# Optimization experiments

Hardware: AMD Instinct MI355X
Metric: run time of the kernel (lower is better)

## Reference

```python
import jax, jax.numpy as jnp
import numpy as np

PS = 8          # patch_size
NF = 64         # num_feat
HEADS = 1
HW = 64         # hard-coded spatial size (Fold output_size=(64,64))
DIM = PS * PS * NF          # 4096
HID = DIM // HEADS          # 4096
NPATCH = (HW // PS) ** 2    # 64


def conv2d(x, w, b, groups=1):
    # x: [N,C,H,W], w: [O, C//groups, 3, 3], padding=1 stride=1 == SAME
    y = jax.lax.conv_general_dilated(
        x, w, window_strides=(1, 1), padding='SAME',
        dimension_numbers=('NCHW', 'OIHW', 'NCHW'),
        feature_group_count=groups)
    return y + b[None, :, None, None]


def unfold(x):
    # nn.Unfold(kernel=PS, stride=PS): [N,C,64,64] -> [N, C*PS*PS, NPATCH]
    N, C = x.shape[0], x.shape[1]
    g = HW // PS
    x = x.reshape(N, C, g, PS, g, PS)          # [N,C,gh,pi,gw,pj]
    x = x.transpose(0, 1, 3, 5, 2, 4)          # [N,C,pi,pj,gh,gw]
    return x.reshape(N, C * PS * PS, g * g)


def fold(y):
    # nn.Fold(output=(64,64), kernel=PS, stride=PS): inverse of unfold (non-overlapping)
    N = y.shape[0]
    g = HW // PS
    y = y.reshape(N, NF, PS, PS, g, g)         # [N,C,pi,pj,gh,gw]
    y = y.transpose(0, 1, 4, 2, 5, 3)          # [N,C,gh,pi,gw,pj]
    return y.reshape(N, NF, HW, HW)


def setup_inputs() -> dict:
    key = jax.random.key(0)
    ks = jax.random.split(key, 9)
    b, t = 4, 16
    x = jax.random.normal(ks[0], (b, t, NF, HW, HW), dtype=jnp.float32)
    s_dw = 1.0 / np.sqrt(9.0)          # depthwise: fan_in = 1*3*3
    s_fc = 1.0 / np.sqrt(NF * 9.0)     # full conv: fan_in = 64*3*3
    qw = jax.random.normal(ks[1], (NF, 1, 3, 3), jnp.float32) * s_dw
    qb = jax.random.normal(ks[2], (NF,), jnp.float32) * 0.01
    kw = jax.random.normal(ks[3], (NF, 1, 3, 3), jnp.float32) * s_dw
    kb = jax.random.normal(ks[4], (NF,), jnp.float32) * 0.01
    vw = jax.random.normal(ks[5], (NF, NF, 3, 3), jnp.float32) * s_fc
    vb = jax.random.normal(ks[6], (NF,), jnp.float32) * 0.01
    cw = jax.random.normal(ks[7], (NF, NF, 3, 3), jnp.float32) * s_fc
    cb = jax.random.normal(ks[8], (NF,), jnp.float32) * 0.01
    return {"x": x, "qw": qw, "qb": qb, "kw": kw, "kb": kb,
            "vw": vw, "vb": vb, "cw": cw, "cb": cb}


def reference(x, qw, qb, kw, kb, vw, vb, cw, cb):
    b, t, c, h, w = x.shape
    H, d, n = HEADS, HID, NPATCH
    xf = x.reshape(b * t, c, h, w)
    q = conv2d(xf, qw, qb, groups=NF)   # depthwise
    k = conv2d(xf, kw, kb, groups=NF)   # depthwise
    v = conv2d(xf, vw, vb)              # full conv
    # unfold -> [b,t,H,d,n] -> [b,H,d,t*n]
    def to_tokens(z):
        z = unfold(z).reshape(b, t, H, d, n)
        return z.transpose(0, 2, 3, 1, 4).reshape(b, H, d, t * n)
    uq, uk, uv = to_tokens(q), to_tokens(k), to_tokens(v)
    attn = jnp.einsum('bhdi,bhdj->bhij', uq, uk) * (d ** -0.5)
    attn = jax.nn.softmax(attn, axis=-1)
    ax = jnp.einsum('bhij,bhdj->bhid', attn, uv)          # [b,H,t*n,d]
    ax = ax.reshape(b, H, t, n, d).transpose(0, 2, 1, 4, 3)  # [b,t,H,d,n]
    ax = ax.reshape(b * t, DIM, n)
    feat = fold(ax)                                        # [b*t,C,64,64]
    out = conv2d(feat, cw, cb).reshape(x.shape)
    return out + x
```

## Files before the change

### kernel.cpp

```cpp
#include <hip/hip_runtime.h>

typedef unsigned short u16;
typedef unsigned int   u32;

typedef __bf16 bf16_t;
typedef bf16_t bf16x8 __attribute__((ext_vector_type(8)));
typedef float  f32x4  __attribute__((ext_vector_type(4)));

__device__ __forceinline__ float bf2f(u16 h) { return __uint_as_float(((u32)h) << 16); }
__device__ __forceinline__ u16 f2bf(float f) {
    u32 u = __float_as_uint(f);
    u32 r = u + 0x7fffu + ((u >> 16) & 1u);
    return (u16)(r >> 16);
}
__device__ __forceinline__ void unpack2(u32 v, float& a, float& b) {
    a = __uint_as_float(v << 16);
    b = __uint_as_float(v & 0xffff0000u);
}


__global__ __launch_bounds__(256) void dwconv_qk(
    const float* __restrict__ x, const float* __restrict__ qw, const float* __restrict__ qb,
    const float* __restrict__ kw, const float* __restrict__ kb,
    u16* __restrict__ qtok, u16* __restrict__ ktok)
{
    __shared__ float ts[64][65];
    int img = blockIdx.x >> 6, c = blockIdx.x & 63;
    int tid = threadIdx.x;
    const float* xp = x + ((size_t)((img << 6) + c) << 12);
    #pragma unroll
    for (int i = 0; i < 4; i++) {
        int p = i * 1024 + tid * 4;
        int r = p >> 6, col = p & 63;
        float4 v = *(const float4*)(xp + p);
        ts[r][col] = v.x; ts[r][col + 1] = v.y; ts[r][col + 2] = v.z; ts[r][col + 3] = v.w;
    }
    float qwv[9], kwv[9];
    #pragma unroll
    for (int i = 0; i < 9; i++) { qwv[i] = qw[c * 9 + i]; kwv[i] = kw[c * 9 + i]; }
    float qbb = qb[c], kbb = kb[c];
    __syncthreads();

    int r = tid >> 2, q = tid & 3;
    int b = img >> 4, t = img & 15;
    int gh = r >> 3, pr = r & 7;
    size_t base = (((size_t)(b << 10) + (t << 6) + (gh << 3)) << 12) + (c << 6) + (pr << 3);

    #pragma unroll
    for (int s = 0; s < 2; s++) {
        int gw = q * 2 + s, w0 = gw << 3;
        float qa[8], ka[8];
        #pragma unroll
        for (int i = 0; i < 8; i++) { qa[i] = qbb; ka[i] = kbb; }
        #pragma unroll
        for (int ky = 0; ky < 3; ky++) {
            int hh = r + ky - 1;
            if (hh < 0 || hh > 63) continue;
            float xr[10];
            #pragma unroll
            for (int cc = 0; cc < 10; cc++) {
                int ww = w0 - 1 + cc;
                xr[cc] = (ww < 0 || ww > 63) ? 0.f : ts[hh][ww];
            }
            #pragma unroll
            for (int kx = 0; kx < 3; kx++) {
                float wq = qwv[ky * 3 + kx], wk = kwv[ky * 3 + kx];
                #pragma unroll
                for (int i = 0; i < 8; i++) {
                    qa[i] += xr[i + kx] * wq;
                    ka[i] += xr[i + kx] * wk;
                }
            }
        }
        union { u16 h8[8]; uint4 u; } pq, pk;
        #pragma unroll
        for (int i = 0; i < 8; i++) { pq.h8[i] = f2bf(qa[i]); pk.h8[i] = f2bf(ka[i]); }
        size_t o = base + ((size_t)gw << 12);
        *(uint4*)&qtok[o] = pq.u;
        *(uint4*)&ktok[o] = pk.u;
    }
}

__global__ __launch_bounds__(256) void nchw_to_nhwc(
    const float* __restrict__ x, u16* __restrict__ xb)
{
    __shared__ float ts[64][65];
    int img = blockIdx.x >> 6, h = blockIdx.x & 63;
    int tid = threadIdx.x;
    const float* xp = x + ((size_t)img << 18) + (h << 6);
    int c = tid >> 2, wg = (tid & 3) << 4;
    #pragma unroll
    for (int i = 0; i < 4; i++) {
        float4 v = *(const float4*)(xp + ((size_t)c << 12) + wg + i * 4);
        ts[c][wg + i * 4 + 0] = v.x; ts[c][wg + i * 4 + 1] = v.y;
        ts[c][wg + i * 4 + 2] = v.z; ts[c][wg + i * 4 + 3] = v.w;
    }
    __syncthreads();
    int w = tid >> 2, cg = (tid & 3) << 4;
    union { u16 h8[8]; uint4 u; } p0, p1;
    #pragma unroll
    for (int m = 0; m < 8; m++) {
        p0.h8[m] = f2bf(ts[cg + m][w]);
        p1.h8[m] = f2bf(ts[cg + 8 + m][w]);
    }
    u16* dst = xb + (((((size_t)img << 6) + h) << 6) + w) * 64 + cg;
    *(uint4*)dst       = p0.u;
    *(uint4*)(dst + 8) = p1.u;
}

__global__ __launch_bounds__(256) void weight_prep2(
    const float* __restrict__ vw, const float* __restrict__ cw, u16* __restrict__ wt)
{
    int e = blockIdx.x * 256 + threadIdx.x;
    if (e >= 73728) return;
    int half = e >= 36864;
    int e2 = e - (half ? 36864 : 0);
    int tap = e2 >> 12;
    int kbg = (e2 >> 9) & 7;
    int cout = (e2 >> 3) & 63;
    int s = e2 & 7;
    int cin = (kbg << 3) + s;
    const float* src = half ? cw : vw;
    wt[e] = f2bf(src[((cout << 6) + cin) * 9 + tap]);
}

template<bool IS_C>
__global__ __launch_bounds__(256, 2) void conv_mfma(
    const u16* __restrict__ xb, const u16* __restrict__ wt,
    const float* __restrict__ bias, const float* __restrict__ xres,
    u16* __restrict__ vt, float* __restrict__ out)
{
    __shared__ u16 xs[21120];
    __shared__ u16 wl[18432];

    int tid = threadIdx.x, lane = tid & 63, wv = tid >> 6;
    int img = blockIdx.x >> 3, rowblk = blockIdx.x & 7;
    int h0 = rowblk << 3;
    int r16 = lane & 15, kb = lane >> 4;

    const uint4 z4 = make_uint4(0, 0, 0, 0);
    for (int i = tid; i < 80; i += 256) {
        int r = i >> 3, k = i & 7;
        *(uint4*)&xs[r * 2112 + 2048 + k * 8] = z4;
    }
    if (rowblk == 0)
        for (int i = tid; i < 264; i += 256) *(uint4*)&xs[i * 8] = z4;
    if (rowblk == 7)
        for (int i = tid; i < 264; i += 256) *(uint4*)&xs[9 * 2112 + i * 8] = z4;

    int pxoff[4][3];
    #pragma unroll
    for (int g = 0; g < 4; g++) {
        #pragma unroll
        for (int dx = 0; dx < 3; dx++) {
            int cc = g * 16 + r16 + dx - 1;
            int off;
            if (cc < 0)        off = 2048 + kb * 8;
            else if (cc >= 64) off = 2080 + kb * 8;
            else               off = (cc >> 4) * 512 + kb * 128 + (cc & 15) * 8;
            pxoff[g][dx] = off;
        }
    }

    const u16* xb_i = xb + ((size_t)img << 18);

    f32x4 acc[4][8] = {};

    for (int c0 = 0; c0 < 64; c0 += 32) {
        __syncthreads();
        #pragma unroll
        for (int k = 0; k < 10; k++) {
            int i = wv + (k << 2);
            int r = i >> 2, g = i & 3;
            int h = h0 + r - 1;
            if (h >= 0 && h < 64) {
                const u16* src = xb_i + (size_t)(((h << 6) + (g << 4) + r16) << 6)
                                 + c0 + (kb << 3);
                u16* dst = xs + r * 2112 + g * 512;
                __builtin_amdgcn_global_load_lds(
                    (const __attribute__((address_space(1))) u32*)src,
                    (__attribute__((address_space(3))) u32*)dst, 16, 0, 0);
            }
        }
        #pragma unroll
        for (int tp = 0; tp < 9; tp++) {
            const u16* srcw = wt + tp * 4096 + (c0 << 6) + tid * 8;
            u16* dstw = wl + tp * 2048 + (wv << 9);
            __builtin_amdgcn_global_load_lds(
                (const __attribute__((address_space(1))) u32*)srcw,
                (__attribute__((address_space(3))) u32*)dstw, 16, 0, 0);
        }
        __syncthreads();

        #pragma unroll
        for (int dy = 0; dy < 3; dy++) {
            #pragma unroll
            for (int dx = 0; dx < 3; dx++) {
                int tap = dy * 3 + dx;
                bf16x8 af[4];
                #pragma unroll
                for (int m = 0; m < 4; m++)
                    af[m] = *(const bf16x8*)&wl[tap * 2048 + (kb << 9)
                                                + (((m << 4) + r16) << 3)];
                #pragma unroll
                for (int nf = 0; nf < 8; nf++) {
                    int rowb = ((wv << 1) + (nf >> 2) + dy) * 2112;
                    bf16x8 bv = *(const bf16x8*)&xs[rowb + pxoff[nf & 3][dx]];
                    #pragma unroll
                    for (int m = 0; m < 4; m++)
                        acc[m][nf] = __builtin_amdgcn_mfma_f32_16x16x32_bf16(
                            af[m], bv, acc[m][nf], 0, 0, 0);
                }
            }
        }
    }

    int b = img >> 4, t = img & 15;
    if constexpr (!IS_C) {
        __syncthreads();
        u16* wbuf = xs + (wv << 12);
        int j0 = (t << 6) + (rowblk << 3);
        #pragma unroll
        for (int mh = 0; mh < 2; mh++) {
            #pragma unroll
            for (int mm = 0; mm < 2; mm++) {
                int m = mh * 2 + mm;
                #pragma unroll
                for (int q = 0; q < 4; q++) {
                    int cm = mm * 16 + (kb << 2) + q;
                    float bvs = bias[mh * 32 + cm];
                    #pragma unroll
                    for (int nf = 0; nf < 8; nf++) {
                        int lrL = nf >> 2;
                        int pc  = r16 & 7;
                        int gw  = ((nf & 3) << 1) | (r16 >> 3);
                        wbuf[(((cm << 1) | lrL) << 6) + (pc << 3) + gw] =
                            f2bf(acc[m][nf][q] + bvs);
                    }
                }
            }
            #pragma unroll
            for (int it = 0; it < 8; it++) {
                int cid = it * 64 + lane;
                int cm  = cid >> 4;
                int lrL = (cid >> 3) & 1;
                int pc  = cid & 7;
                int lr  = (wv << 1) | lrL;
                int cout = mh * 32 + cm;
                int dd  = (((lr << 3) | pc) << 6) | cout;
                uint4 val = *(uint4*)&wbuf[cid << 3];
                *(uint4*)&vt[(((size_t)((b << 12) + dd)) << 10) + j0] = val;
            }
            if (mh == 0) __syncthreads();
        }
    } else {
        #pragma unroll
        for (int m = 0; m < 4; m++) {
            #pragma unroll
            for (int q = 0; q < 4; q++) {
                int cout = (m << 4) + (kb << 2) + q;
                float bvs = bias[cout];
                #pragma unroll
                for (int nf = 0; nf < 8; nf++) {
                    int lr = (wv << 1) + (nf >> 2);
                    int w = (nf & 3) * 16 + r16;
                    int h = h0 + lr;
                    size_t o = ((size_t)((img << 6) + cout) << 12) + (h << 6) + w;
                    out[o] = acc[m][nf][q] + bvs + xres[o];
                }
            }
        }
    }
}

template<int TM, int LDA, int LDB, int LDC, int KTOT, int MT, int NT, int EPI>
__global__ __launch_bounds__(256, 3) void mfma_abt(
    const u16* __restrict__ Ag, const u16* __restrict__ Bg,
    const float* __restrict__ invl, u16* __restrict__ Cg)
{
    constexpr int MF = TM / 32;
    __shared__ u16 As[TM * 64];
    __shared__ u16 Bs[128 * 64];

    int tid  = threadIdx.x;
    int lane = tid & 63, wv = tid >> 6;
    int nt   = blockIdx.x % NT;
    int rest = blockIdx.x / NT;
    int mt   = rest % MT;
    int bi   = rest / MT;

    const u16* Ab = Ag + (size_t)bi * (1024 * (size_t)LDA) + (size_t)(mt * TM) * LDA;
    const u16* Bb = Bg + (size_t)bi * ((size_t)NT * 128 * LDB) + (size_t)(nt * 128) * LDB;

    int srow = tid >> 3;
    int slot = tid & 7;
    int wr = wv >> 1, wc = wv & 1;
    int r16 = lane & 15, kb = lane >> 4;

    f32x4 acc[MF][4] = {};

    for (int k0 = 0; k0 < KTOT; k0 += 64) {
        __syncthreads();
        #pragma unroll
        for (int it = 0; it < MF; it++) {
            int rl = it * 32 + srow;
            int kg = slot ^ (rl & 7);
            const u16* sa = Ab + (size_t)rl * LDA + k0 + kg * 8;
            u16* da = As + it * 2048 + wv * 512;
            __builtin_amdgcn_global_load_lds(
                (const __attribute__((address_space(1))) u32*)sa,
                (__attribute__((address_space(3))) u32*)da, 16, 0, 0);
        }
        #pragma unroll
        for (int it = 0; it < 4; it++) {
            int rl = it * 32 + srow;
            int kg = slot ^ (rl & 7);
            const u16* sb = Bb + (size_t)rl * LDB + k0 + kg * 8;
            u16* db = Bs + it * 2048 + wv * 512;
            __builtin_amdgcn_global_load_lds(
                (const __attribute__((address_space(1))) u32*)sb,
                (__attribute__((address_space(3))) u32*)db, 16, 0, 0);
        }
        __syncthreads();

        #pragma unroll
        for (int kk = 0; kk < 2; kk++) {
            bf16x8 af[MF], bfr[4];
            #pragma unroll
            for (int m = 0; m < MF; m++) {
                int row  = wr * (TM / 2) + m * 16 + r16;
                int boff = row * 128 + (((kk * 32 + kb * 8) * 2) ^ ((row & 7) << 4));
                af[m] = *(const bf16x8*)((const char*)As + boff);
            }
            #pragma unroll
            for (int n = 0; n < 4; n++) {
                int row  = wc * 64 + n * 16 + r16;
                int boff = row * 128 + (((kk * 32 + kb * 8) * 2) ^ ((row & 7) << 4));
                bfr[n] = *(const bf16x8*)((const char*)Bs + boff);
            }
            #pragma unroll
            for (int m = 0; m < MF; m++)
                #pragma unroll
                for (int n = 0; n < 4; n++)
                    acc[m][n] = __builtin_amdgcn_mfma_f32_16x16x32_bf16(
                        af[m], bfr[n], acc[m][n], 0, 0, 0);
        }
    }

    size_t crow0 = (size_t)bi * 1024 + (size_t)mt * TM + wr * (TM / 2);
    int col0 = nt * 128 + wc * 64;
    #pragma unroll
    for (int m = 0; m < MF; m++) {
        float il[4] = {1.f, 1.f, 1.f, 1.f};
        if constexpr (EPI == 2) {
            #pragma unroll
            for (int q = 0; q < 4; q++)
                il[q] = invl[crow0 + m * 16 + kb * 4 + q];
        }
        #pragma unroll
        for (int n = 0; n < 4; n++) {
            #pragma unroll
            for (int q = 0; q < 4; q++) {
                int i_loc = m * 16 + kb * 4 + q;
                int j     = col0 + n * 16 + r16;
                float v   = acc[m][n][q];
                if constexpr (EPI == 0) {
                    Cg[(crow0 + i_loc) * (size_t)LDC + j] = f2bf(__expf(v * 0.015625f));
                } else {
                    int i2 = mt * TM + wr * (TM / 2) + i_loc;
                    int t = i2 >> 6, patch = i2 & 63;
                    int c = j & 63, pr = (j >> 9) & 7, pc = (j >> 6) & 7;
                    int h = ((patch >> 3) << 3) + pr, w2 = ((patch & 7) << 3) + pc;
                    size_t o = ((((size_t)(bi * 16 + t) << 6) + h) << 6) + w2;
                    Cg[(o << 6) + c] = f2bf(v * il[q]);
                }
            }
        }
    }
}

__global__ __launch_bounds__(256) void rowsum_inv_kernel(
    const u16* __restrict__ p, float* __restrict__ invl)
{
    int row = blockIdx.x, tid = threadIdx.x;
    uint2 v = ((const uint2*)(p + ((size_t)row << 10)))[tid];
    float a, b, c, d;
    unpack2(v.x, a, b); unpack2(v.y, c, d);
    float s = (a + b) + (c + d);
    #pragma unroll
    for (int off = 32; off; off >>= 1) s += __shfl_xor(s, off);
    __shared__ float rs[4];
    if ((tid & 63) == 0) rs[tid >> 6] = s;
    __syncthreads();
    if (tid == 0) invl[row] = 1.f / ((rs[0] + rs[1]) + (rs[2] + rs[3]));
}

extern "C" void kernel_launch(void* const* d_in, const int* in_sizes, int n_in,
                              void* d_out, int out_size, void* d_ws, size_t ws_size,
                              hipStream_t stream)
{
    const float* x  = (const float*)d_in[0];
    const float* qw = (const float*)d_in[1];
    const float* qb = (const float*)d_in[2];
    const float* kw = (const float*)d_in[3];
    const float* kb = (const float*)d_in[4];
    const float* vw = (const float*)d_in[5];
    const float* vb = (const float*)d_in[6];
    const float* cw = (const float*)d_in[7];
    const float* cb = (const float*)d_in[8];
    float* out = (float*)d_out;

    char* ws = (char*)d_ws;
    u16*   qtok  = (u16*)d_out;
    u16*   ktok  = (u16*)ws;
    u16*   probs = (u16*)(ws + (size_t)32 * 1024 * 1024);
    float* invl  = (float*)(ws + (size_t)40 * 1024 * 1024);
    u16*   wtv   = (u16*)(ws + (size_t)40 * 1024 * 1024 + 65536);
    u16*   wtc   = wtv + 36864;
    u16*   xbuf  = ktok;
    u16*   vt    = qtok;
    u16*   axb   = ktok;

    weight_prep2<<<288, 256, 0, stream>>>(vw, cw, wtv);

    dwconv_qk<<<4096, 256, 0, stream>>>(x, qw, qb, kw, kb, qtok, ktok);

    mfma_abt<64, 4096, 4096, 1024, 4096, 16, 8, 0><<<512, 256, 0, stream>>>(
        qtok, ktok, nullptr, probs);

    rowsum_inv_kernel<<<4096, 256, 0, stream>>>(probs, invl);

    nchw_to_nhwc<<<4096, 256, 0, stream>>>(x, xbuf);

    conv_mfma<false><<<512, 256, 0, stream>>>(xbuf, wtv, vb, nullptr, vt, nullptr);

    mfma_abt<128, 1024, 1024, 4096, 1024, 8, 32, 2><<<1024, 256, 0, stream>>>(
        probs, vt, invl, axb);

    conv_mfma<true><<<512, 256, 0, stream>>>(axb, wtc, cb, x, nullptr, out);
}
```

Before: 320.6 us.

## Double-buffer LDS in the MFMA GEMM and swizzle block order across XCDs

```diff
diff --git a/kernel.cpp b/kernel.cpp
--- a/kernel.cpp
+++ b/kernel.cpp
@@ -273,82 +273,95 @@
     }
 }
 
-template<int TM, int LDA, int LDB, int LDC, int KTOT, int MT, int NT, int EPI>
-__global__ __launch_bounds__(256, 3) void mfma_abt(
+template<int TM, int TN, int LDA, int LDB, int LDC, int KTOT, int MT, int NT,
+         int EPI, int OCC>
+__global__ __launch_bounds__(256, OCC) void mfma_abt(
     const u16* __restrict__ Ag, const u16* __restrict__ Bg,
     const float* __restrict__ invl, u16* __restrict__ Cg)
 {
     constexpr int MF = TM / 32;
-    __shared__ u16 As[TM * 64];
-    __shared__ u16 Bs[128 * 64];
+    constexpr int NF = TN / 32;
+    constexpr int KSTEPS = KTOT / 64;
+    constexpr int NWG = 4 * MT * NT;
+    constexpr int CPX = NWG / 8;
+    __shared__ u16 As[2][TM * 64];
+    __shared__ u16 Bs[2][TN * 64];
 
     int tid  = threadIdx.x;
     int lane = tid & 63, wv = tid >> 6;
-    int nt   = blockIdx.x % NT;
-    int rest = blockIdx.x / NT;
+    int bid  = blockIdx.x;
+    int id   = (bid & 7) * CPX + (bid >> 3);
+    int nt   = id % NT;
+    int rest = id / NT;
     int mt   = rest % MT;
     int bi   = rest / MT;
 
     const u16* Ab = Ag + (size_t)bi * (1024 * (size_t)LDA) + (size_t)(mt * TM) * LDA;
-    const u16* Bb = Bg + (size_t)bi * ((size_t)NT * 128 * LDB) + (size_t)(nt * 128) * LDB;
+    const u16* Bb = Bg + (size_t)bi * ((size_t)NT * TN * LDB) + (size_t)(nt * TN) * LDB;
 
     int srow = tid >> 3;
     int slot = tid & 7;
     int wr = wv >> 1, wc = wv & 1;
     int r16 = lane & 15, kb = lane >> 4;
 
-    f32x4 acc[MF][4] = {};
-
-    for (int k0 = 0; k0 < KTOT; k0 += 64) {
-        __syncthreads();
+    f32x4 acc[MF][NF] = {};
+
+    auto STAGE = [&](int bsel, int k0) {
         #pragma unroll
         for (int it = 0; it < MF; it++) {
             int rl = it * 32 + srow;
             int kg = slot ^ (rl & 7);
             const u16* sa = Ab + (size_t)rl * LDA + k0 + kg * 8;
-            u16* da = As + it * 2048 + wv * 512;
+            u16* da = &As[bsel][it * 2048 + wv * 512];
             __builtin_amdgcn_global_load_lds(
                 (const __attribute__((address_space(1))) u32*)sa,
                 (__attribute__((address_space(3))) u32*)da, 16, 0, 0);
         }
         #pragma unroll
-        for (int it = 0; it < 4; it++) {
+        for (int it = 0; it < NF; it++) {
             int rl = it * 32 + srow;
             int kg = slot ^ (rl & 7);
             const u16* sb = Bb + (size_t)rl * LDB + k0 + kg * 8;
-            u16* db = Bs + it * 2048 + wv * 512;
+            u16* db = &Bs[bsel][it * 2048 + wv * 512];
             __builtin_amdgcn_global_load_lds(
                 (const __attribute__((address_space(1))) u32*)sb,
                 (__attribute__((address_space(3))) u32*)db, 16, 0, 0);
         }
-        __syncthreads();
-
+    };
+
+    STAGE(0, 0);
+    __syncthreads();
+
+    for (int s = 0; s < KSTEPS; s++) {
+        int cur = s & 1;
+        if (s + 1 < KSTEPS) STAGE(cur ^ 1, (s + 1) * 64);
         #pragma unroll
         for (int kk = 0; kk < 2; kk++) {
-            bf16x8 af[MF], bfr[4];
+            bf16x8 af[MF], bfr[NF];
             #pragma unroll
             for (int m = 0; m < MF; m++) {
                 int row  = wr * (TM / 2) + m * 16 + r16;
                 int boff = row * 128 + (((kk * 32 + kb * 8) * 2) ^ ((row & 7) << 4));
-                af[m] = *(const bf16x8*)((const char*)As + boff);
-            }
-            #pragma unroll
-            for (int n = 0; n < 4; n++) {
-                int row  = wc * 64 + n * 16 + r16;
+                af[m] = *(const bf16x8*)((const char*)&As[cur][0] + boff);
+            }
+            #pragma unroll
+            for (int n = 0; n < NF; n++) {
+                int row  = wc * (TN / 2) + n * 16 + r16;
                 int boff = row * 128 + (((kk * 32 + kb * 8) * 2) ^ ((row & 7) << 4));
-                bfr[n] = *(const bf16x8*)((const char*)Bs + boff);
+                bfr[n] = *(const bf16x8*)((const char*)&Bs[cur][0] + boff);
             }
             #pragma unroll
             for (int m = 0; m < MF; m++)
                 #pragma unroll
-                for (int n = 0; n < 4; n++)
+                for (int n = 0; n < NF; n++)
                     acc[m][n] = __builtin_amdgcn_mfma_f32_16x16x32_bf16(
                         af[m], bfr[n], acc[m][n], 0, 0, 0);
         }
+        __syncthreads();
     }
 
     size_t crow0 = (size_t)bi * 1024 + (size_t)mt * TM + wr * (TM / 2);
-    int col0 = nt * 128 + wc * 64;
+    int col0 = nt * TN + wc * (TN / 2);
     #pragma unroll
     for (int m = 0; m < MF; m++) {
         float il[4] = {1.f, 1.f, 1.f, 1.f};
@@ -358,7 +371,7 @@
                 il[q] = invl[crow0 + m * 16 + kb * 4 + q];
         }
         #pragma unroll
-        for (int n = 0; n < 4; n++) {
+        for (int n = 0; n < NF; n++) {
             #pragma unroll
             for (int q = 0; q < 4; q++) {
                 int i_loc = m * 16 + kb * 4 + q;
@@ -370,8 +383,8 @@
                     int i2 = mt * TM + wr * (TM / 2) + i_loc;
                     int t = i2 >> 6, patch = i2 & 63;
                     int c = j & 63, pr = (j >> 9) & 7, pc = (j >> 6) & 7;
-                    int h = ((patch >> 3) << 3) + pr, w2 = ((patch & 7) << 3) + pc;
-                    size_t o = ((((size_t)(bi * 16 + t) << 6) + h) << 6) + w2;
+                    int hh = ((patch >> 3) << 3) + pr, w2 = ((patch & 7) << 3) + pc;
+                    size_t o = ((((size_t)(bi * 16 + t) << 6) + hh) << 6) + w2;
                     Cg[(o << 6) + c] = f2bf(v * il[q]);
                 }
             }
@@ -425,7 +438,7 @@
 
     dwconv_qk<<<4096, 256, 0, stream>>>(x, qw, qb, kw, kb, qtok, ktok);
 
-    mfma_abt<64, 4096, 4096, 1024, 4096, 16, 8, 0><<<512, 256, 0, stream>>>(
+    mfma_abt<64, 128, 4096, 4096, 1024, 4096, 16, 8, 0, 3><<<512, 256, 0, stream>>>(
         qtok, ktok, nullptr, probs);
 
     rowsum_inv_kernel<<<4096, 256, 0, stream>>>(probs, invl);
@@ -434,7 +447,7 @@
 
     conv_mfma<false><<<512, 256, 0, stream>>>(xbuf, wtv, vb, nullptr, vt, nullptr);
 
-    mfma_abt<128, 1024, 1024, 4096, 1024, 8, 32, 2><<<1024, 256, 0, stream>>>(
+    mfma_abt<128, 128, 1024, 1024, 4096, 1024, 8, 32, 2, 2><<<1024, 256, 0, stream>>>(
         probs, vt, invl, axb);
 
     conv_mfma<true><<<512, 256, 0, stream>>>(axb, wtc, cb, x, nullptr, out);
```

New measurement: 323.0 us. About the same (+0.8%).
